# Optimization experiments

Hardware: AMD Instinct MI355X
Metric: run time of the kernel (lower is better)

## Reference

```python
import jax, jax.numpy as jnp
import numpy as np

N = 100000   # nodes
E = 1600000  # edges (avg degree 16)
F_IN = 256
H = 64
C = 16


def setup_inputs() -> dict:
    key = jax.random.key(0)
    k1, k2, k3, k4 = jax.random.split(key, 4)
    x = jax.random.normal(k1, (N, F_IN), jnp.float32)
    edge_index = jax.random.randint(k2, (2, E), 0, N, jnp.int32)
    W1 = jax.random.normal(k3, (F_IN, H), jnp.float32) * (1.0 / np.sqrt(F_IN))
    b1 = jnp.zeros((H,), jnp.float32)
    W2 = jax.random.normal(k4, (H, C), jnp.float32) * (1.0 / np.sqrt(H))
    b2 = jnp.zeros((C,), jnp.float32)
    return {"x": x, "edge_index": edge_index, "W1": W1, "b1": b1, "W2": W2, "b2": b2}


def _gcn_conv(h_in, src, dst, norm, W, b):
    # linear transform first (GCNConv: lin has no bias), then normalized scatter-add
    h = h_in @ W                                  # [N, out]
    msg = jnp.take(h, src, axis=0) * norm[:, None]  # [E+N, out] gathered + scaled
    out = jax.ops.segment_sum(msg, dst, num_segments=h_in.shape[0])
    return out + b


def reference(x, edge_index, W1, b1, W2, b2):
    num_nodes = x.shape[0]
    # add self-loops (GCNConv default, edge_weight = 1)
    loop = jnp.arange(num_nodes, dtype=edge_index.dtype)
    src = jnp.concatenate([edge_index[0], loop])
    dst = jnp.concatenate([edge_index[1], loop])
    # symmetric normalization D^{-1/2} A D^{-1/2}
    deg = jax.ops.segment_sum(jnp.ones_like(dst, dtype=x.dtype), dst, num_segments=num_nodes)
    dinv = jnp.where(deg > 0, jax.lax.rsqrt(deg), 0.0)
    norm = jnp.take(dinv, src) * jnp.take(dinv, dst)  # [E+N]
    h = jax.nn.relu(_gcn_conv(x, src, dst, norm, W1, b1))
    # dropout is identity in eval mode
    out = _gcn_conv(h, src, dst, norm, W2, b2)
    return jax.nn.log_softmax(out, axis=1)
```

## Files before the change

### kernel.cpp

```cpp
#include <hip/hip_runtime.h>
#include <hip/hip_fp16.h>
#include <math.h>

#define N_NODES 100000
#define N_EDGES 1600000
#define FIN 256
#define NB 196
#define CAP 10240

typedef _Float16 h8 __attribute__((ext_vector_type(8)));
typedef float f4 __attribute__((ext_vector_type(4)));

__global__ __launch_bounds__(256) void k_prepW1(const float* __restrict__ W1, _Float16* __restrict__ Bfrag) {
    int i = blockIdx.x * 256 + threadIdx.x;
    int j = i & 7, lane = (i >> 3) & 63, nt = (i >> 9) & 3, ks = i >> 11;
    int k = ks * 32 + ((lane >> 4) << 3) + j;
    int c = nt * 16 + (lane & 15);
    Bfrag[i] = (_Float16)W1[k * 64 + c];
}

__global__ __launch_bounds__(256) void k_fill_bins(const int* __restrict__ src, const int* __restrict__ dst,
                                                   int* __restrict__ bcur, int* __restrict__ bpack) {
    __shared__ int hist[NB], curs[NB], bstart[NB];
    const int tid = threadIdx.x;
    for (int i = tid; i < NB; i += 256) { hist[i] = 0; curs[i] = 0; }
    __syncthreads();
    const int base = blockIdx.x * 4096;
    int eb[16], ee[16];
    #pragma unroll
    for (int k = 0; k < 16; ++k) {
        int e = base + k * 256 + tid;
        eb[k] = -1;
        if (e < N_EDGES) {
            int s = src[e], d = dst[e];
            int b = d >> 9;
            eb[k] = b;
            ee[k] = ((d & 511) << 17) | s;
            atomicAdd(&hist[b], 1);
        }
    }
    __syncthreads();
    for (int i = tid; i < NB; i += 256)
        if (hist[i] > 0) bstart[i] = i * CAP + atomicAdd(&bcur[i], hist[i]);
    __syncthreads();
    #pragma unroll
    for (int k = 0; k < 16; ++k) {
        if (eb[k] >= 0) {
            int r = atomicAdd(&curs[eb[k]], 1);
            bpack[bstart[eb[k]] + r] = ee[k];
        }
    }
}

__global__ __launch_bounds__(512) void k_sort_bins(const int* __restrict__ bcur,
                                                   const int* __restrict__ bpack,
                                                   int* __restrict__ pack,
                                                   int* __restrict__ starts,
                                                   int* __restrict__ ends,
                                                   float* __restrict__ dinv) {
    __shared__ int hist[512], sd[512], cur[512];
    const int tid = threadIdx.x;
    const int b = blockIdx.x;
    const int node0 = b << 9;
    hist[tid] = 0;
    __syncthreads();
    const int s0 = b * CAP, s1 = s0 + bcur[b];
    for (int i = s0 + tid; i < s1; i += 512) atomicAdd(&hist[bpack[i] >> 17], 1);
    __syncthreads();
    const int deg = hist[tid];
    sd[tid] = deg;
    __syncthreads();
    for (int off = 1; off < 512; off <<= 1) {
        int tv = (tid >= off) ? sd[tid - off] : 0;
        __syncthreads();
        sd[tid] += tv;
        __syncthreads();
    }
    const int excl = sd[tid] - deg;
    const int n = node0 + tid;
    cur[tid] = s0 + excl;
    if (n < N_NODES) {
        starts[n] = s0 + excl;
        ends[n]   = s0 + excl + deg;
        dinv[n] = rsqrtf((float)deg + 1.0f);
    }
    __syncthreads();
    for (int i = s0 + tid; i < s1; i += 512) {
        int v = bpack[i];
        int pos = atomicAdd(&cur[v >> 17], 1);
        pack[pos] = v & 0x1FFFF;
    }
}

__global__ __launch_bounds__(256) void k_gemm1(const float* __restrict__ x,
                                               const _Float16* __restrict__ Bfrag,
                                               const float* __restrict__ dinv,
                                               __half* __restrict__ hh) {
    const int tid = threadIdx.x;
    const int wave = tid >> 6, lane = tid & 63;
    const int lrow = lane & 15;
    const int lk = lane >> 4;
    const int row0 = blockIdx.x * 128 + wave * 16 + lrow;
    const int row1 = row0 + 64;
    const int rc0 = (row0 < N_NODES) ? row0 : (N_NODES - 1);
    const int rc1 = (row1 < N_NODES) ? row1 : (N_NODES - 1);
    const float di0 = dinv[rc0];
    const float di1 = dinv[rc1];
    const float* xp0 = x + (size_t)rc0 * 256 + lk * 8;
    const float* xp1 = x + (size_t)rc1 * 256 + lk * 8;
    const h8* bp = (const h8*)Bfrag + lane;

    f4 accA0 = {0.f,0.f,0.f,0.f}, accA1 = {0.f,0.f,0.f,0.f};
    f4 accA2 = {0.f,0.f,0.f,0.f}, accA3 = {0.f,0.f,0.f,0.f};
    f4 accB0 = {0.f,0.f,0.f,0.f}, accB1 = {0.f,0.f,0.f,0.f};
    f4 accB2 = {0.f,0.f,0.f,0.f}, accB3 = {0.f,0.f,0.f,0.f};

    #pragma unroll 2
    for (int ks = 0; ks < 8; ++ks) {
        f4 a01 = __builtin_nontemporal_load((const f4*)(xp0 + ks * 32));
        f4 a23 = __builtin_nontemporal_load((const f4*)(xp0 + ks * 32 + 4));
        f4 c01 = __builtin_nontemporal_load((const f4*)(xp1 + ks * 32));
        f4 c23 = __builtin_nontemporal_load((const f4*)(xp1 + ks * 32 + 4));
        h8 afA, afB;
        afA[0] = (_Float16)(a01[0] * di0); afA[1] = (_Float16)(a01[1] * di0);
        afA[2] = (_Float16)(a01[2] * di0); afA[3] = (_Float16)(a01[3] * di0);
        afA[4] = (_Float16)(a23[0] * di0); afA[5] = (_Float16)(a23[1] * di0);
        afA[6] = (_Float16)(a23[2] * di0); afA[7] = (_Float16)(a23[3] * di0);
        afB[0] = (_Float16)(c01[0] * di1); afB[1] = (_Float16)(c01[1] * di1);
        afB[2] = (_Float16)(c01[2] * di1); afB[3] = (_Float16)(c01[3] * di1);
        afB[4] = (_Float16)(c23[0] * di1); afB[5] = (_Float16)(c23[1] * di1);
        afB[6] = (_Float16)(c23[2] * di1); afB[7] = (_Float16)(c23[3] * di1);
        h8 b0 = bp[(ks * 4 + 0) * 64];
        h8 b1 = bp[(ks * 4 + 1) * 64];
        h8 b2 = bp[(ks * 4 + 2) * 64];
        h8 b3 = bp[(ks * 4 + 3) * 64];
        accA0 = __builtin_amdgcn_mfma_f32_16x16x32_f16(afA, b0, accA0, 0, 0, 0);
        accB0 = __builtin_amdgcn_mfma_f32_16x16x32_f16(afB, b0, accB0, 0, 0, 0);
        accA1 = __builtin_amdgcn_mfma_f32_16x16x32_f16(afA, b1, accA1, 0, 0, 0);
        accB1 = __builtin_amdgcn_mfma_f32_16x16x32_f16(afB, b1, accB1, 0, 0, 0);
        accA2 = __builtin_amdgcn_mfma_f32_16x16x32_f16(afA, b2, accA2, 0, 0, 0);
        accB2 = __builtin_amdgcn_mfma_f32_16x16x32_f16(afB, b2, accB2, 0, 0, 0);
        accA3 = __builtin_amdgcn_mfma_f32_16x16x32_f16(afA, b3, accA3, 0, 0, 0);
        accB3 = __builtin_amdgcn_mfma_f32_16x16x32_f16(afB, b3, accB3, 0, 0, 0);
    }

    const int orowA = blockIdx.x * 128 + wave * 16 + lk * 4;
    const int orowB = orowA + 64;
    const bool evlane = ((lane & 1) == 0);
#define STORE_TILE(ACC, NT, OR) { \
    _Pragma("unroll") \
    for (int r = 0; r < 4; ++r) { \
        float v = ACC[r]; \
        float o = __shfl_xor(v, 1); \
        int orow = (OR) + r; \
        if (evlane && orow < N_NODES) \
            *(__half2*)&hh[(size_t)orow * 64 + (NT) * 16 + lrow] = __floats2half2_rn(v, o); \
    } }
    STORE_TILE(accA0, 0, orowA)
    STORE_TILE(accA1, 1, orowA)
    STORE_TILE(accA2, 2, orowA)
    STORE_TILE(accA3, 3, orowA)
    STORE_TILE(accB0, 0, orowB)
    STORE_TILE(accB1, 1, orowB)
    STORE_TILE(accB2, 2, orowB)
    STORE_TILE(accB3, 3, orowB)
#undef STORE_TILE
}

__global__ __launch_bounds__(256) void k_agg1_gemm2(const int* __restrict__ starts,
                                                    const int* __restrict__ ends,
                                                    const int* __restrict__ pack,
                                                    const float* __restrict__ dinv,
                                                    const __half* __restrict__ hh,
                                                    const float* __restrict__ b1,
                                                    const float* __restrict__ W2,
                                                    __half* __restrict__ h2h) {
    __shared__ float W2s[64][17];
    __shared__ float h1s[4][64];
    const int tid = threadIdx.x;
    for (int i = tid; i < 64 * 16; i += 256) W2s[i >> 4][i & 15] = W2[i];
    __syncthreads();

    const int wave = tid >> 6;
    const int lane = tid & 63;
    const int node = blockIdx.x * 4 + wave;
    const int e4 = lane >> 4;
    const int l4 = lane & 15;

    const int s0 = starts[node], s1 = ends[node];
    float4 A = {0.f, 0.f, 0.f, 0.f}, B = {0.f, 0.f, 0.f, 0.f};
    int i = s0;
    for (; i + 7 < s1; i += 8) {
        int p0 = __builtin_nontemporal_load(&pack[i + e4]);
        int p1 = __builtin_nontemporal_load(&pack[i + 4 + e4]);
        uint2 r0 = *(const uint2*)(hh + (size_t)p0 * 64 + 4 * l4);
        uint2 r1 = *(const uint2*)(hh + (size_t)p1 * 64 + 4 * l4);
        float2 f00 = __half22float2(*(const __half2*)&r0.x);
        float2 f01 = __half22float2(*(const __half2*)&r0.y);
        float2 f10 = __half22float2(*(const __half2*)&r1.x);
        float2 f11 = __half22float2(*(const __half2*)&r1.y);
        A.x += f00.x; A.y += f00.y; A.z += f01.x; A.w += f01.y;
        B.x += f10.x; B.y += f10.y; B.z += f11.x; B.w += f11.y;
    }
    for (; i + 3 < s1; i += 4) {
        int p = __builtin_nontemporal_load(&pack[i + e4]);
        uint2 r = *(const uint2*)(hh + (size_t)p * 64 + 4 * l4);
        float2 f0 = __half22float2(*(const __half2*)&r.x);
        float2 f1 = __half22float2(*(const __half2*)&r.y);
        A.x += f0.x; A.y += f0.y; A.z += f1.x; A.w += f1.y;
    }
    if (i + e4 < s1) {
        int p = __builtin_nontemporal_load(&pack[i + e4]);
        uint2 r = *(const uint2*)(hh + (size_t)p * 64 + 4 * l4);
        float2 f0 = __half22float2(*(const __half2*)&r.x);
        float2 f1 = __half22float2(*(const __half2*)&r.y);
        A.x += f0.x; A.y += f0.y; A.z += f1.x; A.w += f1.y;
    }
    A.x += B.x; A.y += B.y; A.z += B.z; A.w += B.w;
    A.x += __shfl_xor(A.x, 16); A.y += __shfl_xor(A.y, 16);
    A.z += __shfl_xor(A.z, 16); A.w += __shfl_xor(A.w, 16);
    A.x += __shfl_xor(A.x, 32); A.y += __shfl_xor(A.y, 32);
    A.z += __shfl_xor(A.z, 32); A.w += __shfl_xor(A.w, 32);

    const float di = dinv[node];
    if (lane < 16) {
        uint2 sr = *(const uint2*)(hh + (size_t)node * 64 + 4 * l4);
        float2 sf0 = __half22float2(*(const __half2*)&sr.x);
        float2 sf1 = __half22float2(*(const __half2*)&sr.y);
        h1s[wave][4 * l4 + 0] = fmaxf((A.x + sf0.x) * di + b1[4 * l4 + 0], 0.f);
        h1s[wave][4 * l4 + 1] = fmaxf((A.y + sf0.y) * di + b1[4 * l4 + 1], 0.f);
        h1s[wave][4 * l4 + 2] = fmaxf((A.z + sf1.x) * di + b1[4 * l4 + 2], 0.f);
        h1s[wave][4 * l4 + 3] = fmaxf((A.w + sf1.y) * di + b1[4 * l4 + 3], 0.f);
    }
    const int j = lane >> 4, cc = lane & 15;
    float g = 0.f;
    #pragma unroll
    for (int t = 0; t < 16; ++t) {
        int k = j * 16 + t;
        g = fmaf(h1s[wave][k], W2s[k][cc], g);
    }
    g += __shfl_xor(g, 16);
    g += __shfl_xor(g, 32);
    g *= di;
    float go = __shfl_xor(g, 1);
    if (lane < 16 && (cc & 1) == 0) {
        *(__half2*)&h2h[(size_t)node * 16 + cc] = __floats2half2_rn(g, go);
    }
}

__global__ __launch_bounds__(256) void k_agg2_final(const int* __restrict__ starts,
                                                    const int* __restrict__ ends,
                                                    const int* __restrict__ pack,
                                                    const float* __restrict__ dinv,
                                                    const __half* __restrict__ h2h,
                                                    const float* __restrict__ b2,
                                                    float* __restrict__ out) {
    const int tid = threadIdx.x;
    const int wave = tid >> 6;
    const int lane = tid & 63;
    const int node = blockIdx.x * 4 + wave;
    const int j = lane >> 3, cp = lane & 7;

    const int s0 = starts[node], s1 = ends[node];
    float2 a0 = {0.f, 0.f}, a1 = {0.f, 0.f};
    int i = s0 + j;
    for (; i + 8 < s1; i += 16) {
        int p0 = __builtin_nontemporal_load(&pack[i]);
        int p1 = __builtin_nontemporal_load(&pack[i + 8]);
        float2 f0 = __half22float2(*(const __half2*)(h2h + (size_t)p0 * 16 + 2 * cp));
        float2 f1 = __half22float2(*(const __half2*)(h2h + (size_t)p1 * 16 + 2 * cp));
        a0.x += f0.x; a0.y += f0.y;
        a1.x += f1.x; a1.y += f1.y;
    }
    for (; i < s1; i += 8) {
        int p = __builtin_nontemporal_load(&pack[i]);
        float2 f = __half22float2(*(const __half2*)(h2h + (size_t)p * 16 + 2 * cp));
        a0.x += f.x; a0.y += f.y;
    }
    float2 z;
    z.x = a0.x + a1.x;
    z.y = a0.y + a1.y;
    z.x += __shfl_xor(z.x, 8);  z.y += __shfl_xor(z.y, 8);
    z.x += __shfl_xor(z.x, 16); z.y += __shfl_xor(z.y, 16);
    z.x += __shfl_xor(z.x, 32); z.y += __shfl_xor(z.y, 32);

    const float di = dinv[node];
    float2 sf = __half22float2(*(const __half2*)(h2h + (size_t)node * 16 + 2 * cp));
    z.x = (z.x + sf.x) * di + b2[2 * cp];
    z.y = (z.y + sf.y) * di + b2[2 * cp + 1];

    float m = fmaxf(z.x, z.y);
    m = fmaxf(m, __shfl_xor(m, 1, 8));
    m = fmaxf(m, __shfl_xor(m, 2, 8));
    m = fmaxf(m, __shfl_xor(m, 4, 8));
    float ex = __expf(z.x - m), ey = __expf(z.y - m);
    float s = ex + ey;
    s += __shfl_xor(s, 1, 8);
    s += __shfl_xor(s, 2, 8);
    s += __shfl_xor(s, 4, 8);
    float ls = logf(s);
    if (j == 0) {
        float2 o;
        o.x = z.x - m - ls;
        o.y = z.y - m - ls;
        *(float2*)&out[(size_t)node * 16 + 2 * cp] = o;
    }
}

extern "C" void kernel_launch(void* const* d_in, const int* in_sizes, int n_in,
                              void* d_out, int out_size, void* d_ws, size_t ws_size,
                              hipStream_t stream) {
    const float* x  = (const float*)d_in[0];
    const int* ei   = (const int*)d_in[1];
    const float* W1 = (const float*)d_in[2];
    const float* b1 = (const float*)d_in[3];
    const float* W2 = (const float*)d_in[4];
    const float* b2 = (const float*)d_in[5];
    const int* src = ei;
    const int* dst = ei + N_EDGES;

    _Float16* Bfrag = (_Float16*)d_ws;
    int*    bcur    = (int*)d_ws + 8192;
    int*    starts  = bcur + NB;
    int*    ends    = starts + N_NODES;
    float*  dinv    = (float*)(ends + N_NODES);
    int*    bpack   = (int*)(dinv + N_NODES);
    int*    pack    = bpack + NB * CAP;
    __half* hh      = (__half*)(pack + NB * CAP);
    __half* h2h     = hh + (size_t)N_NODES * 64;
    float*  out     = (float*)d_out;

    hipMemsetAsync(bcur, 0, NB * sizeof(int), stream);

    k_prepW1<<<64, 256, 0, stream>>>(W1, Bfrag);
    k_fill_bins<<<(N_EDGES + 4095) / 4096, 256, 0, stream>>>(src, dst, bcur, bpack);
    k_sort_bins<<<NB, 512, 0, stream>>>(bcur, bpack, pack, starts, ends, dinv);
    k_gemm1<<<(N_NODES + 127) / 128, 256, 0, stream>>>(x, Bfrag, dinv, hh);
    k_agg1_gemm2<<<N_NODES / 4, 256, 0, stream>>>(starts, ends, pack, dinv, hh, b1, W2, h2h);
    k_agg2_final<<<N_NODES / 4, 256, 0, stream>>>(starts, ends, pack, dinv, h2h, b2, out);
}
```

Baseline: 206.0 us.

## Compute degrees up front and co-schedule edge binning with first GEMM

Adds a separate global-atomic degree count and dinv kernel, so the first GEMM no longer has to wait for the bin sort. Edge binning and the x@W1 GEMM then run as two block groups inside one fused launch so they can overlap. Nontemporal loads are replaced with plain loads for x and the pack indices. The cost is an extra pass over dst with 1.6M global atomics, a larger memset, and two more small launches.

```diff
diff --git a/kernel.cpp b/kernel.cpp
--- a/kernel.cpp
+++ b/kernel.cpp
@@ -7,9 +7,20 @@
 #define FIN 256
 #define NB 196
 #define CAP 10240
+#define NFILL 391
+#define NGEMM 782
 
 typedef _Float16 h8 __attribute__((ext_vector_type(8)));
 typedef float f4 __attribute__((ext_vector_type(4)));
+
+__global__ __launch_bounds__(256) void k_count_deg(const int* __restrict__ dst, int* __restrict__ degi) {
+    int e = blockIdx.x * 256 + threadIdx.x;
+    if (e < N_EDGES) atomicAdd(&degi[dst[e]], 1);
+}
+__global__ __launch_bounds__(256) void k_dinv(const int* __restrict__ degi, float* __restrict__ dinv) {
+    int i = blockIdx.x * 256 + threadIdx.x;
+    if (i < N_NODES) dinv[i] = rsqrtf((float)degi[i] + 1.0f);
+}
 
 __global__ __launch_bounds__(256) void k_prepW1(const float* __restrict__ W1, _Float16* __restrict__ Bfrag) {
     int i = blockIdx.x * 256 + threadIdx.x;
@@ -19,36 +30,112 @@
     Bfrag[i] = (_Float16)W1[k * 64 + c];
 }
 
-__global__ __launch_bounds__(256) void k_fill_bins(const int* __restrict__ src, const int* __restrict__ dst,
-                                                   int* __restrict__ bcur, int* __restrict__ bpack) {
-    __shared__ int hist[NB], curs[NB], bstart[NB];
+__global__ __launch_bounds__(256) void k_front(const int* __restrict__ src, const int* __restrict__ dst,
+                                               int* __restrict__ bcur, int* __restrict__ bpack,
+                                               const float* __restrict__ x,
+                                               const _Float16* __restrict__ Bfrag,
+                                               const float* __restrict__ dinv,
+                                               __half* __restrict__ hh) {
     const int tid = threadIdx.x;
-    for (int i = tid; i < NB; i += 256) { hist[i] = 0; curs[i] = 0; }
-    __syncthreads();
-    const int base = blockIdx.x * 4096;
-    int eb[16], ee[16];
-    #pragma unroll
-    for (int k = 0; k < 16; ++k) {
-        int e = base + k * 256 + tid;
-        eb[k] = -1;
-        if (e < N_EDGES) {
-            int s = src[e], d = dst[e];
-            int b = d >> 9;
-            eb[k] = b;
-            ee[k] = ((d & 511) << 17) | s;
-            atomicAdd(&hist[b], 1);
+    if (blockIdx.x < NFILL) {
+        __shared__ int hist[NB], curs[NB], bstart[NB];
+        for (int i = tid; i < NB; i += 256) { hist[i] = 0; curs[i] = 0; }
+        __syncthreads();
+        const int base = blockIdx.x * 4096;
+        int eb[16], ee[16];
+        #pragma unroll
+        for (int k = 0; k < 16; ++k) {
+            int e = base + k * 256 + tid;
+            eb[k] = -1;
+            if (e < N_EDGES) {
+                int s = src[e], d = dst[e];
+                int b = d >> 9;
+                eb[k] = b;
+                ee[k] = ((d & 511) << 17) | s;
+                atomicAdd(&hist[b], 1);
+            }
         }
-    }
-    __syncthreads();
-    for (int i = tid; i < NB; i += 256)
-        if (hist[i] > 0) bstart[i] = i * CAP + atomicAdd(&bcur[i], hist[i]);
-    __syncthreads();
-    #pragma unroll
-    for (int k = 0; k < 16; ++k) {
-        if (eb[k] >= 0) {
-            int r = atomicAdd(&curs[eb[k]], 1);
-            bpack[bstart[eb[k]] + r] = ee[k];
+        __syncthreads();
+        for (int i = tid; i < NB; i += 256)
+            if (hist[i] > 0) bstart[i] = i * CAP + atomicAdd(&bcur[i], hist[i]);
+        __syncthreads();
+        #pragma unroll
+        for (int k = 0; k < 16; ++k) {
+            if (eb[k] >= 0) {
+                int r = atomicAdd(&curs[eb[k]], 1);
+                bpack[bstart[eb[k]] + r] = ee[k];
+            }
         }
+    } else {
+        const int bid = blockIdx.x - NFILL;
+        const int wave = tid >> 6, lane = tid & 63;
+        const int lrow = lane & 15;
+        const int lk = lane >> 4;
+        const int row0 = bid * 128 + wave * 16 + lrow;
+        const int row1 = row0 + 64;
+        const int rc0 = (row0 < N_NODES) ? row0 : (N_NODES - 1);
+        const int rc1 = (row1 < N_NODES) ? row1 : (N_NODES - 1);
+        const float di0 = dinv[rc0];
+        const float di1 = dinv[rc1];
+        const float* xp0 = x + (size_t)rc0 * 256 + lk * 8;
+        const float* xp1 = x + (size_t)rc1 * 256 + lk * 8;
+        const h8* bp = (const h8*)Bfrag + lane;
+
+        f4 accA0 = {0.f,0.f,0.f,0.f}, accA1 = {0.f,0.f,0.f,0.f};
+        f4 accA2 = {0.f,0.f,0.f,0.f}, accA3 = {0.f,0.f,0.f,0.f};
+        f4 accB0 = {0.f,0.f,0.f,0.f}, accB1 = {0.f,0.f,0.f,0.f};
+        f4 accB2 = {0.f,0.f,0.f,0.f}, accB3 = {0.f,0.f,0.f,0.f};
+
+        #pragma unroll 2
+        for (int ks = 0; ks < 8; ++ks) {
+            float4 a01 = *(const float4*)(xp0 + ks * 32);
+            float4 a23 = *(const float4*)(xp0 + ks * 32 + 4);
+            float4 c01 = *(const float4*)(xp1 + ks * 32);
+            float4 c23 = *(const float4*)(xp1 + ks * 32 + 4);
+            h8 afA, afB;
+            afA[0] = (_Float16)(a01.x * di0); afA[1] = (_Float16)(a01.y * di0);
+            afA[2] = (_Float16)(a01.z * di0); afA[3] = (_Float16)(a01.w * di0);
+            afA[4] = (_Float16)(a23.x * di0); afA[5] = (_Float16)(a23.y * di0);
+            afA[6] = (_Float16)(a23.z * di0); afA[7] = (_Float16)(a23.w * di0);
+            afB[0] = (_Float16)(c01.x * di1); afB[1] = (_Float16)(c01.y * di1);
+            afB[2] = (_Float16)(c01.z * di1); afB[3] = (_Float16)(c01.w * di1);
+            afB[4] = (_Float16)(c23.x * di1); afB[5] = (_Float16)(c23.y * di1);
+            afB[6] = (_Float16)(c23.z * di1); afB[7] = (_Float16)(c23.w * di1);
+            h8 b0 = bp[(ks * 4 + 0) * 64];
+            h8 b1 = bp[(ks * 4 + 1) * 64];
+            h8 b2 = bp[(ks * 4 + 2) * 64];
+            h8 b3 = bp[(ks * 4 + 3) * 64];
+            accA0 = __builtin_amdgcn_mfma_f32_16x16x32_f16(afA, b0, accA0, 0, 0, 0);
+            accB0 = __builtin_amdgcn_mfma_f32_16x16x32_f16(afB, b0, accB0, 0, 0, 0);
+            accA1 = __builtin_amdgcn_mfma_f32_16x16x32_f16(afA, b1, accA1, 0, 0, 0);
+            accB1 = __builtin_amdgcn_mfma_f32_16x16x32_f16(afB, b1, accB1, 0, 0, 0);
+            accA2 = __builtin_amdgcn_mfma_f32_16x16x32_f16(afA, b2, accA2, 0, 0, 0);
+            accB2 = __builtin_amdgcn_mfma_f32_16x16x32_f16(afB, b2, accB2, 0, 0, 0);
+            accA3 = __builtin_amdgcn_mfma_f32_16x16x32_f16(afA, b3, accA3, 0, 0, 0);
+            accB3 = __builtin_amdgcn_mfma_f32_16x16x32_f16(afB, b3, accB3, 0, 0, 0);
+        }
+
+        const int orowA = bid * 128 + wave * 16 + lk * 4;
+        const int orowB = orowA + 64;
+        const bool evlane = ((lane & 1) == 0);
+#define STORE_TILE(ACC, NT, OR) { \
+        _Pragma("unroll") \
+        for (int r = 0; r < 4; ++r) { \
+            float v = ACC[r]; \
+            float o = __shfl_xor(v, 1); \
+            int orow = (OR) + r; \
+            if (evlane && orow < N_NODES) \
+                *(__half2*)&hh[(size_t)orow * 64 + (NT) * 16 + lrow] = __floats2half2_rn(v, o); \
+        } }
+        STORE_TILE(accA0, 0, orowA)
+        STORE_TILE(accA1, 1, orowA)
+        STORE_TILE(accA2, 2, orowA)
+        STORE_TILE(accA3, 3, orowA)
+        STORE_TILE(accB0, 0, orowB)
+        STORE_TILE(accB1, 1, orowB)
+        STORE_TILE(accB2, 2, orowB)
+        STORE_TILE(accB3, 3, orowB)
+#undef STORE_TILE
     }
 }
 
@@ -56,8 +143,7 @@
                                                    const int* __restrict__ bpack,
                                                    int* __restrict__ pack,
                                                    int* __restrict__ starts,
-                                                   int* __restrict__ ends,
-                                                   float* __restrict__ dinv) {
+                                                   int* __restrict__ ends) {
     __shared__ int hist[512], sd[512], cur[512];
     const int tid = threadIdx.x;
     const int b = blockIdx.x;
@@ -82,7 +168,6 @@
     if (n < N_NODES) {
         starts[n] = s0 + excl;
         ends[n]   = s0 + excl + deg;
-        dinv[n] = rsqrtf((float)deg + 1.0f);
     }
     __syncthreads();
     for (int i = s0 + tid; i < s1; i += 512) {
@@ -90,81 +175,6 @@
         int pos = atomicAdd(&cur[v >> 17], 1);
         pack[pos] = v & 0x1FFFF;
     }
-}
-
-__global__ __launch_bounds__(256) void k_gemm1(const float* __restrict__ x,
-                                               const _Float16* __restrict__ Bfrag,
-                                               const float* __restrict__ dinv,
-                                               __half* __restrict__ hh) {
-    const int tid = threadIdx.x;
-    const int wave = tid >> 6, lane = tid & 63;
-    const int lrow = lane & 15;
-    const int lk = lane >> 4;
-    const int row0 = blockIdx.x * 128 + wave * 16 + lrow;
-    const int row1 = row0 + 64;
-    const int rc0 = (row0 < N_NODES) ? row0 : (N_NODES - 1);
-    const int rc1 = (row1 < N_NODES) ? row1 : (N_NODES - 1);
-    const float di0 = dinv[rc0];
-    const float di1 = dinv[rc1];
-    const float* xp0 = x + (size_t)rc0 * 256 + lk * 8;
-    const float* xp1 = x + (size_t)rc1 * 256 + lk * 8;
-    const h8* bp = (const h8*)Bfrag + lane;
-
-    f4 accA0 = {0.f,0.f,0.f,0.f}, accA1 = {0.f,0.f,0.f,0.f};
-    f4 accA2 = {0.f,0.f,0.f,0.f}, accA3 = {0.f,0.f,0.f,0.f};
-    f4 accB0 = {0.f,0.f,0.f,0.f}, accB1 = {0.f,0.f,0.f,0.f};
-    f4 accB2 = {0.f,0.f,0.f,0.f}, accB3 = {0.f,0.f,0.f,0.f};
-
-    #pragma unroll 2
-    for (int ks = 0; ks < 8; ++ks) {
-        f4 a01 = __builtin_nontemporal_load((const f4*)(xp0 + ks * 32));
-        f4 a23 = __builtin_nontemporal_load((const f4*)(xp0 + ks * 32 + 4));
-        f4 c01 = __builtin_nontemporal_load((const f4*)(xp1 + ks * 32));
-        f4 c23 = __builtin_nontemporal_load((const f4*)(xp1 + ks * 32 + 4));
-        h8 afA, afB;
-        afA[0] = (_Float16)(a01[0] * di0); afA[1] = (_Float16)(a01[1] * di0);
-        afA[2] = (_Float16)(a01[2] * di0); afA[3] = (_Float16)(a01[3] * di0);
-        afA[4] = (_Float16)(a23[0] * di0); afA[5] = (_Float16)(a23[1] * di0);
-        afA[6] = (_Float16)(a23[2] * di0); afA[7] = (_Float16)(a23[3] * di0);
-        afB[0] = (_Float16)(c01[0] * di1); afB[1] = (_Float16)(c01[1] * di1);
-        afB[2] = (_Float16)(c01[2] * di1); afB[3] = (_Float16)(c01[3] * di1);
-        afB[4] = (_Float16)(c23[0] * di1); afB[5] = (_Float16)(c23[1] * di1);
-        afB[6] = (_Float16)(c23[2] * di1); afB[7] = (_Float16)(c23[3] * di1);
-        h8 b0 = bp[(ks * 4 + 0) * 64];
-        h8 b1 = bp[(ks * 4 + 1) * 64];
-        h8 b2 = bp[(ks * 4 + 2) * 64];
-        h8 b3 = bp[(ks * 4 + 3) * 64];
-        accA0 = __builtin_amdgcn_mfma_f32_16x16x32_f16(afA, b0, accA0, 0, 0, 0);
-        accB0 = __builtin_amdgcn_mfma_f32_16x16x32_f16(afB, b0, accB0, 0, 0, 0);
-        accA1 = __builtin_amdgcn_mfma_f32_16x16x32_f16(afA, b1, accA1, 0, 0, 0);
-        accB1 = __builtin_amdgcn_mfma_f32_16x16x32_f16(afB, b1, accB1, 0, 0, 0);
-        accA2 = __builtin_amdgcn_mfma_f32_16x16x32_f16(afA, b2, accA2, 0, 0, 0);
-        accB2 = __builtin_amdgcn_mfma_f32_16x16x32_f16(afB, b2, accB2, 0, 0, 0);
-        accA3 = __builtin_amdgcn_mfma_f32_16x16x32_f16(afA, b3, accA3, 0, 0, 0);
-        accB3 = __builtin_amdgcn_mfma_f32_16x16x32_f16(afB, b3, accB3, 0, 0, 0);
-    }
-
-    const int orowA = blockIdx.x * 128 + wave * 16 + lk * 4;
-    const int orowB = orowA + 64;
-    const bool evlane = ((lane & 1) == 0);
-#define STORE_TILE(ACC, NT, OR) { \
-    _Pragma("unroll") \
-    for (int r = 0; r < 4; ++r) { \
-        float v = ACC[r]; \
-        float o = __shfl_xor(v, 1); \
-        int orow = (OR) + r; \
-        if (evlane && orow < N_NODES) \
-            *(__half2*)&hh[(size_t)orow * 64 + (NT) * 16 + lrow] = __floats2half2_rn(v, o); \
-    } }
-    STORE_TILE(accA0, 0, orowA)
-    STORE_TILE(accA1, 1, orowA)
-    STORE_TILE(accA2, 2, orowA)
-    STORE_TILE(accA3, 3, orowA)
-    STORE_TILE(accB0, 0, orowB)
-    STORE_TILE(accB1, 1, orowB)
-    STORE_TILE(accB2, 2, orowB)
-    STORE_TILE(accB3, 3, orowB)
-#undef STORE_TILE
 }
 
 __global__ __launch_bounds__(256) void k_agg1_gemm2(const int* __restrict__ starts,
@@ -191,8 +201,7 @@
     float4 A = {0.f, 0.f, 0.f, 0.f}, B = {0.f, 0.f, 0.f, 0.f};
     int i = s0;
     for (; i + 7 < s1; i += 8) {
-        int p0 = __builtin_nontemporal_load(&pack[i + e4]);
-        int p1 = __builtin_nontemporal_load(&pack[i + 4 + e4]);
+        int p0 = pack[i + e4], p1 = pack[i + 4 + e4];
         uint2 r0 = *(const uint2*)(hh + (size_t)p0 * 64 + 4 * l4);
         uint2 r1 = *(const uint2*)(hh + (size_t)p1 * 64 + 4 * l4);
         float2 f00 = __half22float2(*(const __half2*)&r0.x);
@@ -203,14 +212,14 @@
         B.x += f10.x; B.y += f10.y; B.z += f11.x; B.w += f11.y;
     }
     for (; i + 3 < s1; i += 4) {
-        int p = __builtin_nontemporal_load(&pack[i + e4]);
+        int p = pack[i + e4];
         uint2 r = *(const uint2*)(hh + (size_t)p * 64 + 4 * l4);
         float2 f0 = __half22float2(*(const __half2*)&r.x);
         float2 f1 = __half22float2(*(const __half2*)&r.y);
         A.x += f0.x; A.y += f0.y; A.z += f1.x; A.w += f1.y;
     }
     if (i + e4 < s1) {
-        int p = __builtin_nontemporal_load(&pack[i + e4]);
+        int p = pack[i + e4];
         uint2 r = *(const uint2*)(hh + (size_t)p * 64 + 4 * l4);
         float2 f0 = __half22float2(*(const __half2*)&r.x);
         float2 f1 = __half22float2(*(const __half2*)&r.y);
@@ -265,15 +274,14 @@
     float2 a0 = {0.f, 0.f}, a1 = {0.f, 0.f};
     int i = s0 + j;
     for (; i + 8 < s1; i += 16) {
-        int p0 = __builtin_nontemporal_load(&pack[i]);
-        int p1 = __builtin_nontemporal_load(&pack[i + 8]);
+        int p0 = pack[i], p1 = pack[i + 8];
         float2 f0 = __half22float2(*(const __half2*)(h2h + (size_t)p0 * 16 + 2 * cp));
         float2 f1 = __half22float2(*(const __half2*)(h2h + (size_t)p1 * 16 + 2 * cp));
         a0.x += f0.x; a0.y += f0.y;
         a1.x += f1.x; a1.y += f1.y;
     }
     for (; i < s1; i += 8) {
-        int p = __builtin_nontemporal_load(&pack[i]);
+        int p = pack[i];
         float2 f = __half22float2(*(const __half2*)(h2h + (size_t)p * 16 + 2 * cp));
         a0.x += f.x; a0.y += f.y;
     }
@@ -321,7 +329,8 @@
 
     _Float16* Bfrag = (_Float16*)d_ws;
     int*    bcur    = (int*)d_ws + 8192;
-    int*    starts  = bcur + NB;
+    int*    degi    = bcur + NB;
+    int*    starts  = degi + N_NODES;
     int*    ends    = starts + N_NODES;
     float*  dinv    = (float*)(ends + N_NODES);
     int*    bpack   = (int*)(dinv + N_NODES);
@@ -330,12 +339,13 @@
     __half* h2h     = hh + (size_t)N_NODES * 64;
     float*  out     = (float*)d_out;
 
-    hipMemsetAsync(bcur, 0, NB * sizeof(int), stream);
-
+    hipMemsetAsync(bcur, 0, (NB + N_NODES) * sizeof(int), stream);
+
+    k_count_deg<<<(N_EDGES + 255) / 256, 256, 0, stream>>>(dst, degi);
+    k_dinv<<<(N_NODES + 255) / 256, 256, 0, stream>>>(degi, dinv);
     k_prepW1<<<64, 256, 0, stream>>>(W1, Bfrag);
-    k_fill_bins<<<(N_EDGES + 4095) / 4096, 256, 0, stream>>>(src, dst, bcur, bpack);
-    k_sort_bins<<<NB, 512, 0, stream>>>(bcur, bpack, pack, starts, ends, dinv);
-    k_gemm1<<<(N_NODES + 127) / 128, 256, 0, stream>>>(x, Bfrag, dinv, hh);
+    k_front<<<NFILL + NGEMM, 256, 0, stream>>>(src, dst, bcur, bpack, x, Bfrag, dinv, hh);
+    k_sort_bins<<<NB, 512, 0, stream>>>(bcur, bpack, pack, starts, ends);
     k_agg1_gemm2<<<N_NODES / 4, 256, 0, stream>>>(starts, ends, pack, dinv, hh, b1, W2, h2h);
     k_agg2_final<<<N_NODES / 4, 256, 0, stream>>>(starts, ends, pack, dinv, h2h, b2, out);
 }
```

Result: slower. 236.3 us (+14.7%).
